# Kernel tuning notes

Measured on AMD Instinct MI355X. Metric: run time of the kernel, lower is better.

## Reference

```python
import jax, jax.numpy as jnp
import numpy as np

B, T, V, H, L = 128, 512, 256, 512, 2  # batch, seq, vocab, hidden, layers


def setup_inputs() -> dict:
    key = jax.random.key(0)
    ks = jax.random.split(key, 12)
    s = 0.05
    p = lambda k, shape: (jax.random.normal(k, shape, jnp.float32) * s)
    return {
        "x": jax.random.normal(ks[0], (B, T, V), jnp.float32),
        # layer 0 (input size V)
        "w_ih0": p(ks[1], (4 * H, V)),
        "w_hh0": p(ks[2], (4 * H, H)),
        "b_ih0": p(ks[3], (4 * H,)),
        "b_hh0": p(ks[4], (4 * H,)),
        # layer 1 (input size H)
        "w_ih1": p(ks[5], (4 * H, H)),
        "w_hh1": p(ks[6], (4 * H, H)),
        "b_ih1": p(ks[7], (4 * H,)),
        "b_hh1": p(ks[8], (4 * H,)),
        # final projection
        "fc_w": p(ks[9], (V, H)),
        "fc_b": p(ks[10], (V,)),
    }


def _lstm_layer(x, w_ih, w_hh, b_ih, b_hh):
    """x: [B,T,in] -> (outputs [B,T,H], h_T [B,H], c_T [B,H]). PyTorch gate order i,f,g,o."""
    Bb = x.shape[0]
    Hh = w_hh.shape[1]
    # precompute input contribution for all timesteps: [B,T,4H]
    pre = jnp.einsum('bti,gi->btg', x, w_ih) + b_ih + b_hh

    def step(carry, xt):
        h, c = carry
        gates = xt + h @ w_hh.T  # [B,4H]
        i, f, g, o = jnp.split(gates, 4, axis=-1)
        i = jax.nn.sigmoid(i)
        f = jax.nn.sigmoid(f)
        g = jnp.tanh(g)
        o = jax.nn.sigmoid(o)
        c = f * c + i * g
        h = o * jnp.tanh(c)
        return (h, c), h

    h0 = jnp.zeros((Bb, Hh), x.dtype)
    (hT, cT), hs = jax.lax.scan(step, (h0, h0), jnp.swapaxes(pre, 0, 1))
    return jnp.swapaxes(hs, 0, 1), hT, cT


def reference(x, w_ih0, w_hh0, b_ih0, b_hh0, w_ih1, w_hh1, b_ih1, b_hh1, fc_w, fc_b):
    out0, h0, c0 = _lstm_layer(x, w_ih0, w_hh0, b_ih0, b_hh0)
    out1, h1, c1 = _lstm_layer(out0, w_ih1, w_hh1, b_ih1, b_hh1)
    last = out1[:, -1, :]                # slice final timestep [B,H]
    # dropout is identity in eval mode
    logits = last @ fc_w.T + fc_b        # [B,V]
    h_n = jnp.stack([h0, h1])            # [L,B,H]
    c_n = jnp.stack([c0, c1])
    return (logits, h_n, c_n)
```

## Files before the change

kernel.cpp:

```cpp
#include <hip/hip_runtime.h>
#include <math.h>

#define B_ 128
#define T_ 512
#define V_ 256
#define H_ 512

typedef unsigned short u16;
typedef unsigned int u32;
typedef unsigned long long u64;
typedef __attribute__((ext_vector_type(8))) __bf16 bf16x8;
typedef __attribute__((ext_vector_type(4))) float f32x4;
typedef __attribute__((ext_vector_type(4))) u32 u32x4;

__device__ __forceinline__ float sigf(float x) { return 1.f / (1.f + __expf(-x)); }
__device__ __forceinline__ float tanh_fast(float x) {
    x = fminf(fmaxf(x, -15.f), 15.f);
    float e = __expf(2.f * x);
    return (e - 1.f) / (e + 1.f);
}
__device__ __forceinline__ u16 f2bf(float f) {
    union { float f; u32 u; } v; v.f = f;
    u32 r = v.u + 0x7FFFu + ((v.u >> 16) & 1u);
    return (u16)(r >> 16);
}

__device__ __forceinline__ u64 aload(const u64* p) {
    return __hip_atomic_load(p, __ATOMIC_RELAXED, __HIP_MEMORY_SCOPE_AGENT);
}
__device__ __forceinline__ void astore(u64* p, u64 v) {
    __hip_atomic_store(p, v, __ATOMIC_RELAXED, __HIP_MEMORY_SCOPE_AGENT);
}
__device__ __forceinline__ u32 aload32(const u32* p) {
    return __hip_atomic_load(p, __ATOMIC_RELAXED, __HIP_MEMORY_SCOPE_AGENT);
}
__device__ __forceinline__ void astore32(u32* p, u32 v) {
    __hip_atomic_store(p, v, __ATOMIC_RELAXED, __HIP_MEMORY_SCOPE_AGENT);
}
__device__ __forceinline__ void pollge(const u32* slots, int idx, int target) {
    const u32* p = slots + idx;
    for (;;) {
        u32 v = aload32(p);
        if (__all((int)v >= target)) break;
        __builtin_amdgcn_s_sleep(1);
    }
    __builtin_amdgcn_sched_barrier(0);
    asm volatile("" ::: "memory");
}
__device__ __forceinline__ bf16x8 afrag(const u16* p) {
    union { u64 d[2]; bf16x8 v; } u;
    u.d[0] = aload((const u64*)p);
    u.d[1] = aload((const u64*)(p + 4));
    return u.v;
}

__global__ __launch_bounds__(256) void conv_x(u16* __restrict__ dst, const float* __restrict__ x) {
    int tid = blockIdx.x * 256 + threadIdx.x;
    int k = tid & (V_ - 1);
    int t = (tid >> 8) & (T_ - 1);
    int b = tid >> 17;
    float v = x[tid];
    int lane = (b & 15) | (((k >> 3) & 3) << 4);
    dst[((((size_t)t * 8 + (b >> 4)) * 8) + (k >> 5)) * 512 + (size_t)lane * 8 + (k & 7)] = f2bf(v);
}

__global__ __launch_bounds__(256) void conv_w(u16* __restrict__ dst,
                                              const float* __restrict__ wih,
                                              const float* __restrict__ whh,
                                              int KIN, int Ktot) {
    int tid = blockIdx.x * 256 + threadIdx.x;
    int n = tid / Ktot, k = tid - n * Ktot;
    float v = (k < KIN) ? wih[(size_t)n * KIN + k] : whh[(size_t)n * H_ + (k - KIN)];
    int lane = (n & 15) | (((k >> 3) & 3) << 4);
    dst[((size_t)((n >> 4) * (Ktot >> 5) + (k >> 5))) * 512 + (size_t)lane * 8 + (k & 7)] = f2bf(v);
}

__global__ __launch_bounds__(256) void vadd(float* __restrict__ d,
                                            const float* __restrict__ a,
                                            const float* __restrict__ b, int n) {
    int i = blockIdx.x * 256 + threadIdx.x;
    if (i < n) d[i] = a[i] + b[i];
}


template <int LAYER>
__device__ __forceinline__ void run_loop(
    const u16* __restrict__ Xswz, u16* __restrict__ Out0,
    const u16* __restrict__ WBs,
    f32x4* __restrict__ scr,
    u16* __restrict__ tileb,
    volatile u32* __restrict__ mbox,
    u32* __restrict__ Hgrp,
    const float* __restrict__ bsum, float* __restrict__ out,
    u32* __restrict__ bc,
    int js, int mq, int wid, int lane)
{
    constexpr int KCA = LAYER ? 16 : 8;
    constexpr int KCT = KCA + 16;
    const int m = wid & 1;
    const bool isA = wid < 2;
    const int jl = (js << 4) | (lane & 15);

    if (isA) {
        for (int tc = 0; tc < T_; ++tc) {
            while ((int)mbox[2 + m] < tc - 1) __builtin_amdgcn_s_sleep(1);
            __builtin_amdgcn_sched_barrier(0);
            asm volatile("" ::: "memory");

            f32x4 acc[4];
            #pragma unroll
            for (int g = 0; g < 4; ++g) acc[g] = (f32x4){0.f, 0.f, 0.f, 0.f};
            if (LAYER == 0) {
                const u16* As = Xswz + (size_t)tc * 32768 + (size_t)(2 * mq + m) * 4096 + (size_t)lane * 8;
                #pragma unroll
                for (int kc = 0; kc < 8; ++kc) {
                    bf16x8 a = *(const bf16x8*)(As + (size_t)kc * 512);
                    #pragma unroll
                    for (int g = 0; g < 4; ++g)
                        acc[g] = __builtin_amdgcn_mfma_f32_16x16x32_bf16(
                            a, *(const bf16x8*)(WBs + (size_t)(g * KCT + kc) * 512 + (size_t)lane * 8), acc[g], 0, 0, 0);
                }
            } else {
                pollge(bc + m * 32, lane & 31, tc + 1);
                const u16* As = Out0 + (size_t)tc * 65536 + (size_t)(2 * mq + m) * 8192 + (size_t)lane * 8;
                bf16x8 fa[16];
                #pragma unroll
                for (int kc = 0; kc < 16; ++kc) fa[kc] = afrag(As + (size_t)kc * 512);
                #pragma unroll
                for (int kc = 0; kc < 16; ++kc) {
                    #pragma unroll
                    for (int g = 0; g < 4; ++g)
                        acc[g] = __builtin_amdgcn_mfma_f32_16x16x32_bf16(
                            fa[kc], *(const bf16x8*)(WBs + (size_t)(g * KCT + kc) * 512 + (size_t)lane * 8), acc[g], 0, 0, 0);
                }
            }
            #pragma unroll
            for (int g = 0; g < 4; ++g) scr[(size_t)(((tc & 1) * 2 + m) * 4 + g) * 64 + lane] = acc[g];
            asm volatile("s_waitcnt lgkmcnt(0)" ::: "memory");
            if (lane == 0) mbox[m] = (u32)(tc + 1);
        }
    } else {
        const float bi0 = bsum[jl], bi1 = bsum[512 + jl];
        const float bi2 = bsum[1024 + jl], bi3 = bsum[1536 + jl];
        f32x4 creg = {0.f, 0.f, 0.f, 0.f};
        u32* bcs = bc + m * 32 + js;

        for (int s = 0; s < T_; ++s) {
            const u32 tag = (u32)s;
            const u32* hb = Hgrp + (size_t)(s & 1) * 16384 + (size_t)m * 8192;
            u64 fA[16], fB[16];
            #pragma unroll
            for (int i = 0; i < 16; ++i)
                fA[i] = aload((const u64*)(hb + (size_t)(i >> 2) * 512 + (size_t)lane * 8) + (i & 3));

            while ((int)mbox[m] < s + 1) __builtin_amdgcn_s_sleep(1);
            __builtin_amdgcn_sched_barrier(0);
            asm volatile("" ::: "memory");
            f32x4 acc[4];
            #pragma unroll
            for (int g = 0; g < 4; ++g) acc[g] = scr[(size_t)(((s & 1) * 2 + m) * 4 + g) * 64 + lane];
            asm volatile("s_waitcnt lgkmcnt(0)" ::: "memory");
            if (lane == 0) mbox[2 + m] = (u32)(s + 1);

            #pragma unroll
            for (int c = 0; c < 4; ++c) {
                u64* cur = (c & 1) ? fB : fA;
                u64* nxt = (c & 1) ? fA : fB;
                if (c < 3) {
                    #pragma unroll
                    for (int i = 0; i < 16; ++i)
                        nxt[i] = aload((const u64*)(hb + (size_t)((c + 1) * 4 + (i >> 2)) * 512 + (size_t)lane * 8) + (i & 3));
                }
                for (;;) {
                    u32 bad = 0u;
                    #pragma unroll
                    for (int i = 0; i < 16; ++i) bad |= (((u32)(cur[i] >> 16)) & 0xFFFFu) ^ tag;
                    if (!__any(bad != 0u)) break;
                    #pragma unroll
                    for (int i = 0; i < 16; ++i)
                        cur[i] = aload((const u64*)(hb + (size_t)(c * 4 + (i >> 2)) * 512 + (size_t)lane * 8) + (i & 3));
                }
                #pragma unroll
                for (int k2 = 0; k2 < 4; ++k2) {
                    const u64 g0 = cur[4 * k2 + 0], g1 = cur[4 * k2 + 1];
                    const u64 g2 = cur[4 * k2 + 2], g3 = cur[4 * k2 + 3];
                    u32 w0 = (u32)(g0 & 0xFFFFu) | ((u32)(g0 >> 32) << 16);
                    u32 w1 = (u32)(g1 & 0xFFFFu) | ((u32)(g1 >> 32) << 16);
                    u32 w2 = (u32)(g2 & 0xFFFFu) | ((u32)(g2 >> 32) << 16);
                    u32 w3 = (u32)(g3 & 0xFFFFu) | ((u32)(g3 >> 32) << 16);
                    u32x4 ww = {w0, w1, w2, w3};
                    bf16x8 a = __builtin_bit_cast(bf16x8, ww);
                    const int kc = 4 * c + k2;
                    #pragma unroll
                    for (int g = 0; g < 4; ++g)
                        acc[g] = __builtin_amdgcn_mfma_f32_16x16x32_bf16(
                            a, *(const bf16x8*)(WBs + (size_t)(g * KCT + KCA + kc) * 512 + (size_t)lane * 8), acc[g], 0, 0, 0);
                }
            }

            if (LAYER == 0 && s >= 1 && lane == 0) astore32(bcs, (u32)s);

            const bool is_last = (s == T_ - 1);
            const int bb = (lane >> 4) << 2;
            #pragma unroll
            for (int r = 0; r < 4; ++r) {
                const float vi = sigf(acc[0][r] + bi0);
                const float vf = sigf(acc[1][r] + bi1);
                const float vg = tanh_fast(acc[2][r] + bi2);
                const float vo = sigf(acc[3][r] + bi3);
                const float cn = vf * creg[r] + vi * vg;
                creg[r] = cn;
                const float hn = vo * tanh_fast(cn);
                tileb[(size_t)(m * 16 + bb + r) * 20 + (lane & 15)] = f2bf(hn);
                if (is_last) {
                    const int bg = mq * 32 + m * 16 + bb + r;
                    out[(LAYER ? 98304 : 32768) + bg * 512 + jl] = hn;
                    out[(LAYER ? 229376 : 163840) + bg * 512 + jl] = cn;
                }
            }
            const u32 wtag = (u32)(s + 1);
            u32* hw = Hgrp + (size_t)((s + 1) & 1) * 16384 + (size_t)m * 8192;
            #pragma unroll
            for (int q = 0; q < 2; ++q) {
                u32 w = *(const u32*)&tileb[(size_t)(m * 16 + (lane >> 2)) * 20 + q * 8 + (lane & 3) * 2];
                u64 v = (u64)(w & 0xFFFFu) | ((u64)wtag << 16)
                      | ((u64)(w >> 16) << 32) | ((u64)wtag << 48);
                astore((u64*)(hw + (size_t)(js >> 1) * 512 + (size_t)((js & 1) * 2 + q) * 128
                              + (size_t)(lane >> 2) * 8 + (size_t)((lane & 3) * 2)), v);
            }
            if (LAYER == 0) {
                const int q2 = lane >> 5, lw = lane & 31, b2 = lw >> 1, e4 = (lw & 1) * 4;
                u64 v = *(const u64*)&tileb[(size_t)(m * 16 + b2) * 20 + q2 * 8 + e4];
                astore((u64*)(Out0 + (size_t)s * 65536 + (size_t)(2 * mq + m) * 8192
                              + (size_t)(js >> 1) * 512 + (size_t)((js & 1) * 2 + q2) * 128
                              + (size_t)b2 * 8 + (size_t)e4), v);
            }
        }
        if (LAYER == 0) {
            asm volatile("s_waitcnt vmcnt(0)" ::: "memory");
            if (lane == 0) astore32(bcs, (u32)(T_ + 1));
        }
    }
}

__global__ __launch_bounds__(256, 1) void lstm_persistent(
    const u16* __restrict__ Xswz, u16* __restrict__ Out0swz,
    const u16* __restrict__ WB0, const u16* __restrict__ WB1,
    const float* __restrict__ bsum0, const float* __restrict__ bsum1,
    u32* __restrict__ Htag, float* __restrict__ out, u32* __restrict__ bc)
{
    __shared__ u16 WBs[4 * 32 * 512];
    __shared__ f32x4 scr[2 * 2 * 4 * 64];
    __shared__ __align__(16) u16 tileb[2 * 16 * 20];
    __shared__ u32 mbox[4];

    const int bid = blockIdx.x;
    const int g = bid & 7, js = bid >> 3;
    const int layer = g >> 2, mq = g & 3;
    const int tid = threadIdx.x;
    const int wid = tid >> 6, lane = tid & 63;

    const int KCtot = layer ? 32 : 24;
    const u16* WB = layer ? WB1 : WB0;
    for (int gg = 0; gg < 4; ++gg) {
        const u32x4* s4 = (const u32x4*)(WB + ((size_t)(gg * 32 + js) * KCtot) * 512);
        u32x4* d4 = (u32x4*)(WBs + (size_t)gg * KCtot * 512);
        for (int i = tid; i < KCtot * 64; i += 256) d4[i] = s4[i];
    }
    if (tid < 4) mbox[tid] = 0u;
    __syncthreads();

    u32* Hgrp = Htag + (size_t)g * 32768;
    u32* bcg = bc + mq * 64;

    if (layer == 0)
        run_loop<0>(Xswz, Out0swz, WBs, scr, tileb, mbox, Hgrp, bsum0, out, bcg, js, mq, wid, lane);
    else
        run_loop<1>(Xswz, Out0swz, WBs, scr, tileb, mbox, Hgrp, bsum1, out, bcg, js, mq, wid, lane);
}

__device__ __forceinline__ float dot4_(float4 a, float4 w, float s) {
    s = fmaf(a.x, w.x, s); s = fmaf(a.y, w.y, s);
    s = fmaf(a.z, w.z, s); s = fmaf(a.w, w.w, s);
    return s;
}

__global__ __launch_bounds__(256) void logits_kernel(
    const float* __restrict__ h1, const float* __restrict__ fc_w,
    const float* __restrict__ fc_b, float* __restrict__ out)
{
    __shared__ float hs[H_];
    const int b = blockIdx.x;
    for (int k = threadIdx.x; k < H_; k += 256) hs[k] = h1[(size_t)b * H_ + k];
    __syncthreads();
    const int v = threadIdx.x;
    const float4* wr = reinterpret_cast<const float4*>(fc_w + (size_t)v * H_);
    const float4* hr = reinterpret_cast<const float4*>(hs);
    float s = 0.f;
    #pragma unroll 8
    for (int k = 0; k < H_ / 4; ++k) s = dot4_(hr[k], wr[k], s);
    out[(size_t)b * V_ + v] = s + fc_b[v];
}

extern "C" void kernel_launch(void* const* d_in, const int* in_sizes, int n_in,
                              void* d_out, int out_size, void* d_ws, size_t ws_size,
                              hipStream_t stream) {
    const float* x     = (const float*)d_in[0];
    const float* w_ih0 = (const float*)d_in[1];
    const float* w_hh0 = (const float*)d_in[2];
    const float* b_ih0 = (const float*)d_in[3];
    const float* b_hh0 = (const float*)d_in[4];
    const float* w_ih1 = (const float*)d_in[5];
    const float* w_hh1 = (const float*)d_in[6];
    const float* b_ih1 = (const float*)d_in[7];
    const float* b_hh1 = (const float*)d_in[8];
    const float* fc_w  = (const float*)d_in[9];
    const float* fc_b  = (const float*)d_in[10];
    float* out = (float*)d_out;

    char* p = (char*)d_ws;
    u16* Xswz    = (u16*)p; p += (size_t)512 * 32768 * 2;
    u16* Out0swz = (u16*)p; p += (size_t)512 * 65536 * 2;
    u16* WB0     = (u16*)p; p += (size_t)128 * 24 * 512 * 2;
    u16* WB1     = (u16*)p; p += (size_t)128 * 32 * 512 * 2;
    u32* Htag    = (u32*)p; p += (size_t)8 * 32768 * 4;
    float* bsum0 = (float*)p; p += 2048 * 4;
    float* bsum1 = (float*)p; p += 2048 * 4;
    u32* bc      = (u32*)p;  p += 4 * 64 * 4;

    hipMemsetAsync(Htag, 0, (size_t)8 * 32768 * 4, stream);
    hipMemsetAsync(bc, 0, 4 * 64 * 4, stream);
    conv_x<<<65536, 256, 0, stream>>>(Xswz, x);
    conv_w<<<(2048 * 768) / 256, 256, 0, stream>>>(WB0, w_ih0, w_hh0, 256, 768);
    conv_w<<<(2048 * 1024) / 256, 256, 0, stream>>>(WB1, w_ih1, w_hh1, 512, 1024);
    vadd<<<8, 256, 0, stream>>>(bsum0, b_ih0, b_hh0, 2048);
    vadd<<<8, 256, 0, stream>>>(bsum1, b_ih1, b_hh1, 2048);

    lstm_persistent<<<256, 256, 0, stream>>>(
        Xswz, Out0swz, WB0, WB1, bsum0, bsum1, Htag, out, bc);

    logits_kernel<<<B_, 256, 0, stream>>>(out + 98304, fc_w, fc_b, out);
}
```

Measured before the change: 3.132 ms.

## Replace LDS mailbox spin handshakes with barriers and inline layer-0 input projection

Removes the shared-memory mailbox protocol between producer and consumer warps. In layer 0 the recurrent warps now compute the input projection themselves and the producer warps exit. In layer 1 the producer and consumer warps hand off the precomputed gates through `__syncthreads` instead of sleep-polled counters. The first hidden-state fragment load for the next step is now issued at the end of each iteration. The aim is to cut spin and sleep latency on the serial recurrence. The cost is that layer 0 now does its input MFMAs on the critical path, and layer 1 producers are coupled to consumers by a full block barrier every step.

```diff
diff --git a/kernel.cpp b/kernel.cpp
--- a/kernel.cpp
+++ b/kernel.cpp
@@ -89,7 +89,6 @@
     const u16* __restrict__ WBs,
     f32x4* __restrict__ scr,
     u16* __restrict__ tileb,
-    volatile u32* __restrict__ mbox,
     u32* __restrict__ Hgrp,
     const float* __restrict__ bsum, float* __restrict__ out,
     u32* __restrict__ bc,
@@ -102,144 +101,151 @@
     const int jl = (js << 4) | (lane & 15);
 
     if (isA) {
+        if (LAYER == 0) return;
         for (int tc = 0; tc < T_; ++tc) {
-            while ((int)mbox[2 + m] < tc - 1) __builtin_amdgcn_s_sleep(1);
-            __builtin_amdgcn_sched_barrier(0);
-            asm volatile("" ::: "memory");
-
+            pollge(bc + m * 32, lane & 31, tc + 1);
+            const u16* As = Out0 + (size_t)tc * 65536 + (size_t)(2 * mq + m) * 8192 + (size_t)lane * 8;
             f32x4 acc[4];
             #pragma unroll
             for (int g = 0; g < 4; ++g) acc[g] = (f32x4){0.f, 0.f, 0.f, 0.f};
-            if (LAYER == 0) {
-                const u16* As = Xswz + (size_t)tc * 32768 + (size_t)(2 * mq + m) * 4096 + (size_t)lane * 8;
-                #pragma unroll
-                for (int kc = 0; kc < 8; ++kc) {
-                    bf16x8 a = *(const bf16x8*)(As + (size_t)kc * 512);
-                    #pragma unroll
-                    for (int g = 0; g < 4; ++g)
-                        acc[g] = __builtin_amdgcn_mfma_f32_16x16x32_bf16(
-                            a, *(const bf16x8*)(WBs + (size_t)(g * KCT + kc) * 512 + (size_t)lane * 8), acc[g], 0, 0, 0);
-                }
-            } else {
-                pollge(bc + m * 32, lane & 31, tc + 1);
-                const u16* As = Out0 + (size_t)tc * 65536 + (size_t)(2 * mq + m) * 8192 + (size_t)lane * 8;
-                bf16x8 fa[16];
-                #pragma unroll
-                for (int kc = 0; kc < 16; ++kc) fa[kc] = afrag(As + (size_t)kc * 512);
-                #pragma unroll
-                for (int kc = 0; kc < 16; ++kc) {
-                    #pragma unroll
-                    for (int g = 0; g < 4; ++g)
-                        acc[g] = __builtin_amdgcn_mfma_f32_16x16x32_bf16(
-                            fa[kc], *(const bf16x8*)(WBs + (size_t)(g * KCT + kc) * 512 + (size_t)lane * 8), acc[g], 0, 0, 0);
-                }
+            bf16x8 fa[16];
+            #pragma unroll
+            for (int kc = 0; kc < 16; ++kc) fa[kc] = afrag(As + (size_t)kc * 512);
+            #pragma unroll
+            for (int kc = 0; kc < 16; ++kc) {
+                #pragma unroll
+                for (int g = 0; g < 4; ++g)
+                    acc[g] = __builtin_amdgcn_mfma_f32_16x16x32_bf16(
+                        fa[kc], *(const bf16x8*)(WBs + (size_t)(g * KCT + kc) * 512 + (size_t)lane * 8), acc[g], 0, 0, 0);
             }
             #pragma unroll
             for (int g = 0; g < 4; ++g) scr[(size_t)(((tc & 1) * 2 + m) * 4 + g) * 64 + lane] = acc[g];
-            asm volatile("s_waitcnt lgkmcnt(0)" ::: "memory");
-            if (lane == 0) mbox[m] = (u32)(tc + 1);
-        }
-    } else {
-        const float bi0 = bsum[jl], bi1 = bsum[512 + jl];
-        const float bi2 = bsum[1024 + jl], bi3 = bsum[1536 + jl];
-        f32x4 creg = {0.f, 0.f, 0.f, 0.f};
-        u32* bcs = bc + m * 32 + js;
-
-        for (int s = 0; s < T_; ++s) {
-            const u32 tag = (u32)s;
-            const u32* hb = Hgrp + (size_t)(s & 1) * 16384 + (size_t)m * 8192;
-            u64 fA[16], fB[16];
+            __syncthreads();
+        }
+        return;
+    }
+
+    const float bi0 = bsum[jl], bi1 = bsum[512 + jl];
+    const float bi2 = bsum[1024 + jl], bi3 = bsum[1536 + jl];
+    f32x4 creg = {0.f, 0.f, 0.f, 0.f};
+    u32* bcs = bc + m * 32 + js;
+
+    u64 fA[16], fB[16];
+    {
+        const u32* hb0 = Hgrp + (size_t)m * 8192;
+        #pragma unroll
+        for (int i = 0; i < 16; ++i)
+            fA[i] = aload((const u64*)(hb0 + (size_t)(i >> 2) * 512 + (size_t)lane * 8) + (i & 3));
+    }
+
+    for (int s = 0; s < T_; ++s) {
+        const u32 tag = (u32)s;
+        const u32* hb = Hgrp + (size_t)(s & 1) * 16384 + (size_t)m * 8192;
+
+        f32x4 acc[4];
+        if (LAYER == 0) {
+            #pragma unroll
+            for (int g = 0; g < 4; ++g) acc[g] = (f32x4){0.f, 0.f, 0.f, 0.f};
+            const u16* As = Xswz + (size_t)s * 32768 + (size_t)(2 * mq + m) * 4096 + (size_t)lane * 8;
+            #pragma unroll
+            for (int kc = 0; kc < 8; ++kc) {
+                bf16x8 a = *(const bf16x8*)(As + (size_t)kc * 512);
+                #pragma unroll
+                for (int g = 0; g < 4; ++g)
+                    acc[g] = __builtin_amdgcn_mfma_f32_16x16x32_bf16(
+                        a, *(const bf16x8*)(WBs + (size_t)(g * KCT + kc) * 512 + (size_t)lane * 8), acc[g], 0, 0, 0);
+            }
+        } else {
+            __syncthreads();
+            #pragma unroll
+            for (int g = 0; g < 4; ++g) acc[g] = scr[(size_t)(((s & 1) * 2 + m) * 4 + g) * 64 + lane];
+        }
+
+        #pragma unroll
+        for (int c = 0; c < 4; ++c) {
+            u64* cur = (c & 1) ? fB : fA;
+            u64* nxt = (c & 1) ? fA : fB;
+            if (c < 3) {
+                #pragma unroll
+                for (int i = 0; i < 16; ++i)
+                    nxt[i] = aload((const u64*)(hb + (size_t)((c + 1) * 4 + (i >> 2)) * 512 + (size_t)lane * 8) + (i & 3));
+            }
+            for (;;) {
+                u32 bad = 0u;
+                #pragma unroll
+                for (int i = 0; i < 16; ++i) bad |= (((u32)(cur[i] >> 16)) & 0xFFFFu) ^ tag;
+                if (!__any(bad != 0u)) break;
+                #pragma unroll
+                for (int i = 0; i < 16; ++i)
+                    cur[i] = aload((const u64*)(hb + (size_t)(c * 4 + (i >> 2)) * 512 + (size_t)lane * 8) + (i & 3));
+            }
+            #pragma unroll
+            for (int k2 = 0; k2 < 4; ++k2) {
+                const u64 g0 = cur[4 * k2 + 0], g1 = cur[4 * k2 + 1];
+                const u64 g2 = cur[4 * k2 + 2], g3 = cur[4 * k2 + 3];
+                u32 w0 = (u32)(g0 & 0xFFFFu) | ((u32)(g0 >> 32) << 16);
+                u32 w1 = (u32)(g1 & 0xFFFFu) | ((u32)(g1 >> 32) << 16);
+                u32 w2 = (u32)(g2 & 0xFFFFu) | ((u32)(g2 >> 32) << 16);
+                u32 w3 = (u32)(g3 & 0xFFFFu) | ((u32)(g3 >> 32) << 16);
+                u32x4 ww = {w0, w1, w2, w3};
+                bf16x8 a = __builtin_bit_cast(bf16x8, ww);
+                const int kc = 4 * c + k2;
+                #pragma unroll
+                for (int g = 0; g < 4; ++g)
+                    acc[g] = __builtin_amdgcn_mfma_f32_16x16x32_bf16(
+                        a, *(const bf16x8*)(WBs + (size_t)(g * KCT + KCA + kc) * 512 + (size_t)lane * 8), acc[g], 0, 0, 0);
+            }
+        }
+
+        if (LAYER == 0 && s >= 1 && lane == 0) astore32(bcs, (u32)s);
+
+        const bool is_last = (s == T_ - 1);
+        const int bb = (lane >> 4) << 2;
+        #pragma unroll
+        for (int r = 0; r < 4; ++r) {
+            const float vi = sigf(acc[0][r] + bi0);
+            const float vf = sigf(acc[1][r] + bi1);
+            const float vg = tanh_fast(acc[2][r] + bi2);
+            const float vo = sigf(acc[3][r] + bi3);
+            const float cn = vf * creg[r] + vi * vg;
+            creg[r] = cn;
+            const float hn = vo * tanh_fast(cn);
+            tileb[(size_t)(m * 16 + bb + r) * 20 + (lane & 15)] = f2bf(hn);
+            if (is_last) {
+                const int bg = mq * 32 + m * 16 + bb + r;
+                out[(LAYER ? 98304 : 32768) + bg * 512 + jl] = hn;
+                out[(LAYER ? 229376 : 163840) + bg * 512 + jl] = cn;
+            }
+        }
+        const u32 wtag = (u32)(s + 1);
+        u32* hw = Hgrp + (size_t)((s + 1) & 1) * 16384 + (size_t)m * 8192;
+        #pragma unroll
+        for (int q = 0; q < 2; ++q) {
+            u32 w = *(const u32*)&tileb[(size_t)(m * 16 + (lane >> 2)) * 20 + q * 8 + (lane & 3) * 2];
+            u64 v = (u64)(w & 0xFFFFu) | ((u64)wtag << 16)
+                  | ((u64)(w >> 16) << 32) | ((u64)wtag << 48);
+            astore((u64*)(hw + (size_t)(js >> 1) * 512 + (size_t)((js & 1) * 2 + q) * 128
+                          + (size_t)(lane >> 2) * 8 + (size_t)((lane & 3) * 2)), v);
+        }
+        if (LAYER == 0) {
+            const int q2 = lane >> 5, lw = lane & 31, b2 = lw >> 1, e4 = (lw & 1) * 4;
+            u64 v = *(const u64*)&tileb[(size_t)(m * 16 + b2) * 20 + q2 * 8 + e4];
+            astore((u64*)(Out0 + (size_t)s * 65536 + (size_t)(2 * mq + m) * 8192
+                          + (size_t)(js >> 1) * 512 + (size_t)((js & 1) * 2 + q2) * 128
+                          + (size_t)b2 * 8 + (size_t)e4), v);
+        }
+
+        if (s + 1 < T_) {
+            const u32* hbn = Hgrp + (size_t)((s + 1) & 1) * 16384 + (size_t)m * 8192;
             #pragma unroll
             for (int i = 0; i < 16; ++i)
-                fA[i] = aload((const u64*)(hb + (size_t)(i >> 2) * 512 + (size_t)lane * 8) + (i & 3));
-
-            while ((int)mbox[m] < s + 1) __builtin_amdgcn_s_sleep(1);
-            __builtin_amdgcn_sched_barrier(0);
-            asm volatile("" ::: "memory");
-            f32x4 acc[4];
-            #pragma unroll
-            for (int g = 0; g < 4; ++g) acc[g] = scr[(size_t)(((s & 1) * 2 + m) * 4 + g) * 64 + lane];
-            asm volatile("s_waitcnt lgkmcnt(0)" ::: "memory");
-            if (lane == 0) mbox[2 + m] = (u32)(s + 1);
-
-            #pragma unroll
-            for (int c = 0; c < 4; ++c) {
-                u64* cur = (c & 1) ? fB : fA;
-                u64* nxt = (c & 1) ? fA : fB;
-                if (c < 3) {
-                    #pragma unroll
-                    for (int i = 0; i < 16; ++i)
-                        nxt[i] = aload((const u64*)(hb + (size_t)((c + 1) * 4 + (i >> 2)) * 512 + (size_t)lane * 8) + (i & 3));
-                }
-                for (;;) {
-                    u32 bad = 0u;
-                    #pragma unroll
-                    for (int i = 0; i < 16; ++i) bad |= (((u32)(cur[i] >> 16)) & 0xFFFFu) ^ tag;
-                    if (!__any(bad != 0u)) break;
-                    #pragma unroll
-                    for (int i = 0; i < 16; ++i)
-                        cur[i] = aload((const u64*)(hb + (size_t)(c * 4 + (i >> 2)) * 512 + (size_t)lane * 8) + (i & 3));
-                }
-                #pragma unroll
-                for (int k2 = 0; k2 < 4; ++k2) {
-                    const u64 g0 = cur[4 * k2 + 0], g1 = cur[4 * k2 + 1];
-                    const u64 g2 = cur[4 * k2 + 2], g3 = cur[4 * k2 + 3];
-                    u32 w0 = (u32)(g0 & 0xFFFFu) | ((u32)(g0 >> 32) << 16);
-                    u32 w1 = (u32)(g1 & 0xFFFFu) | ((u32)(g1 >> 32) << 16);
-                    u32 w2 = (u32)(g2 & 0xFFFFu) | ((u32)(g2 >> 32) << 16);
-                    u32 w3 = (u32)(g3 & 0xFFFFu) | ((u32)(g3 >> 32) << 16);
-                    u32x4 ww = {w0, w1, w2, w3};
-                    bf16x8 a = __builtin_bit_cast(bf16x8, ww);
-                    const int kc = 4 * c + k2;
-                    #pragma unroll
-                    for (int g = 0; g < 4; ++g)
-                        acc[g] = __builtin_amdgcn_mfma_f32_16x16x32_bf16(
-                            a, *(const bf16x8*)(WBs + (size_t)(g * KCT + KCA + kc) * 512 + (size_t)lane * 8), acc[g], 0, 0, 0);
-                }
-            }
-
-            if (LAYER == 0 && s >= 1 && lane == 0) astore32(bcs, (u32)s);
-
-            const bool is_last = (s == T_ - 1);
-            const int bb = (lane >> 4) << 2;
-            #pragma unroll
-            for (int r = 0; r < 4; ++r) {
-                const float vi = sigf(acc[0][r] + bi0);
-                const float vf = sigf(acc[1][r] + bi1);
-                const float vg = tanh_fast(acc[2][r] + bi2);
-                const float vo = sigf(acc[3][r] + bi3);
-                const float cn = vf * creg[r] + vi * vg;
-                creg[r] = cn;
-                const float hn = vo * tanh_fast(cn);
-                tileb[(size_t)(m * 16 + bb + r) * 20 + (lane & 15)] = f2bf(hn);
-                if (is_last) {
-                    const int bg = mq * 32 + m * 16 + bb + r;
-                    out[(LAYER ? 98304 : 32768) + bg * 512 + jl] = hn;
-                    out[(LAYER ? 229376 : 163840) + bg * 512 + jl] = cn;
-                }
-            }
-            const u32 wtag = (u32)(s + 1);
-            u32* hw = Hgrp + (size_t)((s + 1) & 1) * 16384 + (size_t)m * 8192;
-            #pragma unroll
-            for (int q = 0; q < 2; ++q) {
-                u32 w = *(const u32*)&tileb[(size_t)(m * 16 + (lane >> 2)) * 20 + q * 8 + (lane & 3) * 2];
-                u64 v = (u64)(w & 0xFFFFu) | ((u64)wtag << 16)
-                      | ((u64)(w >> 16) << 32) | ((u64)wtag << 48);
-                astore((u64*)(hw + (size_t)(js >> 1) * 512 + (size_t)((js & 1) * 2 + q) * 128
-                              + (size_t)(lane >> 2) * 8 + (size_t)((lane & 3) * 2)), v);
-            }
-            if (LAYER == 0) {
-                const int q2 = lane >> 5, lw = lane & 31, b2 = lw >> 1, e4 = (lw & 1) * 4;
-                u64 v = *(const u64*)&tileb[(size_t)(m * 16 + b2) * 20 + q2 * 8 + e4];
-                astore((u64*)(Out0 + (size_t)s * 65536 + (size_t)(2 * mq + m) * 8192
-                              + (size_t)(js >> 1) * 512 + (size_t)((js & 1) * 2 + q2) * 128
-                              + (size_t)b2 * 8 + (size_t)e4), v);
-            }
-        }
-        if (LAYER == 0) {
-            asm volatile("s_waitcnt vmcnt(0)" ::: "memory");
-            if (lane == 0) astore32(bcs, (u32)(T_ + 1));
-        }
+                fA[i] = aload((const u64*)(hbn + (size_t)(i >> 2) * 512 + (size_t)lane * 8) + (i & 3));
+        }
+    }
+
+    if (LAYER == 0) {
+        asm volatile("s_waitcnt vmcnt(0)" ::: "memory");
+        if (lane == 0) astore32(bcs, (u32)(T_ + 1));
     }
 }
 
@@ -252,7 +258,6 @@
     __shared__ u16 WBs[4 * 32 * 512];
     __shared__ f32x4 scr[2 * 2 * 4 * 64];
     __shared__ __align__(16) u16 tileb[2 * 16 * 20];
-    __shared__ u32 mbox[4];
 
     const int bid = blockIdx.x;
     const int g = bid & 7, js = bid >> 3;
@@ -267,16 +272,15 @@
         u32x4* d4 = (u32x4*)(WBs + (size_t)gg * KCtot * 512);
         for (int i = tid; i < KCtot * 64; i += 256) d4[i] = s4[i];
     }
-    if (tid < 4) mbox[tid] = 0u;
     __syncthreads();
 
     u32* Hgrp = Htag + (size_t)g * 32768;
     u32* bcg = bc + mq * 64;
 
     if (layer == 0)
-        run_loop<0>(Xswz, Out0swz, WBs, scr, tileb, mbox, Hgrp, bsum0, out, bcg, js, mq, wid, lane);
+        run_loop<0>(Xswz, Out0swz, WBs, scr, tileb, Hgrp, bsum0, out, bcg, js, mq, wid, lane);
     else
-        run_loop<1>(Xswz, Out0swz, WBs, scr, tileb, mbox, Hgrp, bsum1, out, bcg, js, mq, wid, lane);
+        run_loop<1>(Xswz, Out0swz, WBs, scr, tileb, Hgrp, bsum1, out, bcg, js, mq, wid, lane);
 }
 
 __device__ __forceinline__ float dot4_(float4 a, float4 w, float s) {
```

After: 3.054 ms. 2.5% less time.
